# Optimization experiments

Hardware: AMD Instinct MI355X
Metric: run time of the kernel (lower is better)

Reference implementation:

```python
import jax, jax.numpy as jnp
import numpy as np

MAX_SPIKE_TIME = 100.0
TH = 1.0
BIT = 8
K = 3
PAD = 1
OUT_CH = 64


def _unfold3x3(x):
    # torch F.unfold(kernel=3, padding=1, stride=1): output (B, C*9, H*W),
    # feature order channel-major then (kh, kw).
    B, C, H, W = x.shape
    xp = jnp.pad(x, ((0, 0), (0, 0), (PAD, PAD), (PAD, PAD)))
    cols = [xp[:, :, i:i + H, j:j + W] for i in range(K) for j in range(K)]
    p = jnp.stack(cols, axis=2)            # (B, C, 9, H, W)
    return p.reshape(B, C * K * K, H * W)  # (B, C*9, L)


def _weight_quantization(w):
    # tanh -> scale by global abs-max (no grad through alpha) -> round with STE
    w = jnp.tanh(w)
    alpha = jax.lax.stop_gradient(jnp.max(jnp.abs(w)))
    qmax = float(2 ** (BIT - 1) - 1)
    w = jnp.clip(w / alpha, -1.0, 1.0) * qmax
    w_hat = jax.lax.stop_gradient(jnp.round(w) - w) + w
    return w_hat * alpha / qmax


def _t_linear_c(patches, weight):
    # patches: (B, L, F_in); weight: (F_out, F_in)
    sorted_inp = jnp.sort(patches, axis=-1)      # (B, L, F_in)
    indic = jnp.argsort(patches, axis=-1)        # (B, L, F_in)
    wT = weight.T                                # (F_in, F_out)
    w_sorted = wT[indic]                         # (B, L, F_in, F_out)
    wq = _weight_quantization(w_sorted)
    si = sorted_inp[..., None]                   # (B, L, F_in, 1)
    weight_input_mul = si * wq
    weight_sum = jnp.cumsum(wq, axis=-2)
    input_weight_sum = jnp.cumsum(weight_input_mul, axis=-2)
    out_all = input_weight_sum / jnp.clip(weight_sum - TH, 1e-10, 1e10)
    out_spike = jnp.where(weight_sum < TH, MAX_SPIKE_TIME, out_all)
    out_spike = jnp.where(out_spike < si, MAX_SPIKE_TIME, out_spike)
    # causality check against the NEXT sorted input time (1.0 for the last slot)
    next_in = jnp.concatenate([si[..., 1:, :], jnp.ones_like(si[..., :1, :])], axis=-2)
    out_spike = jnp.where(out_spike > next_in, MAX_SPIKE_TIME, out_spike)
    return jnp.min(out_spike, axis=-2)           # (B, L, F_out)


def setup_inputs() -> dict:
    key = jax.random.key(0)
    k1, k2 = jax.random.split(key)
    inp = jax.random.uniform(k1, (4, 16, 32, 32), dtype=jnp.float32)
    in_features = K * K * 16
    weight = jax.random.uniform(k2, (OUT_CH, in_features), dtype=jnp.float32) * (10.0 / in_features)
    return {"inp": inp, "weight": weight}


def reference(inp, weight):
    B, C, H, W = inp.shape
    patches = _unfold3x3(inp).transpose(0, 2, 1)          # (B, L, F_in)
    patches = jnp.where(patches < 0.1, MAX_SPIKE_TIME, patches)
    out = _t_linear_c(patches, weight)                    # (B, L, F_out)
    out = out.transpose(0, 2, 1).reshape(B, OUT_CH, H, W)  # stride=1, pad=1 -> same HW
    return out
```

## Files before the change

kernel.cpp:

```cpp
#include <hip/hip_runtime.h>
#include <math.h>

constexpr int F_IN   = 144;
constexpr int F_OUT  = 64;
constexpr int H_IMG  = 32;
constexpr int W_IMG  = 32;
constexpr int NPIX   = 4 * H_IMG * W_IMG;
constexpr int PPB    = 8;
constexpr int NTHR   = PPB * 64;
#define MAX_SPIKE 100.0f

__global__ __launch_bounds__(256) void quant_fused_kernel(
    const float* __restrict__ w,
    float* __restrict__ wqT)
{
#pragma clang fp contract(off)
    __shared__ float wred[4];
    const int tid = threadIdx.x;

    float m = 0.f;
    {
        const float4* w4 = (const float4*)w;
        for (int i = tid; i < (F_OUT * F_IN) / 4; i += 256) {
            const float4 v = w4[i];
            m = fmaxf(m, fmaxf(fmaxf(fabsf(v.x), fabsf(v.y)),
                               fmaxf(fabsf(v.z), fabsf(v.w))));
        }
    }
    for (int s = 32; s > 0; s >>= 1)
        m = fmaxf(m, __shfl_xor(m, s, 64));
    if ((tid & 63) == 0) wred[tid >> 6] = m;
    __syncthreads();
    const float mw = fmaxf(fmaxf(wred[0], wred[1]), fmaxf(wred[2], wred[3]));
    const float alpha = tanhf(mw);

    const int i = blockIdx.x * 256 + tid;
    const int o = i / F_IN;
    const int f = i - o * F_IN;
    const float t = tanhf(w[i]);
    float x = t / alpha;
    x = fminf(fmaxf(x, -1.f), 1.f) * 127.f;
    const float r = rintf(x);
    wqT[f * F_OUT + o] = r * alpha / 127.f;
}

__global__ __launch_bounds__(NTHR, 4) void spike_conv_kernel(
    const float* __restrict__ inp,
    const float* __restrict__ wq,
    float* __restrict__ out)
{
#pragma clang fp contract(off)
    __shared__ __align__(16) float wql[F_IN * F_OUT];
    __shared__ __align__(16) unsigned long long kr[PPB][F_IN];
    __shared__ float sv[PPB][F_IN + 1];

    const int tid  = threadIdx.x;
    const int lane = tid & 63;
    const int wv_i = tid >> 6;
    const int p    = blockIdx.x * PPB + wv_i;
    const int b    = p >> 10;
    const int l    = p & 1023;
    const int h    = l >> 5;
    const int w    = l & 31;

    for (int c = wv_i; c < 36; c += PPB) {
        const float* g = wq + c * 256 + lane * 4;
        __builtin_amdgcn_global_load_lds(
            (const __attribute__((address_space(1))) void*)g,
            (__attribute__((address_space(3))) void*)&wql[c * 256],
            16, 0, 0);
    }

    float v0f, v1f, v2f;
    unsigned long long key0, key1, key2;
    {
        int idx[3] = { lane, lane + 64, lane + 128 };
        float vals[3];
        for (int m = 0; m < 3; ++m) {
            const int i = idx[m];
            float v = MAX_SPIKE;
            if (i < F_IN) {
                const int c  = i / 9;
                const int r  = i - c * 9;
                const int kh = r / 3;
                const int kw = r - kh * 3;
                const int hh = h + kh - 1;
                const int ww = w + kw - 1;
                float x = 0.f;
                if (hh >= 0 && hh < H_IMG && ww >= 0 && ww < W_IMG)
                    x = inp[((b * 16 + c) * H_IMG + hh) * W_IMG + ww];
                v = (x < 0.1f) ? MAX_SPIKE : x;
                kr[wv_i][i] = ((unsigned long long)__float_as_uint(v) << 8)
                              | (unsigned)i;
            }
            vals[m] = v;
        }
        v0f = vals[0]; v1f = vals[1]; v2f = vals[2];
        key0 = ((unsigned long long)__float_as_uint(v0f) << 8) | (unsigned)idx[0];
        key1 = ((unsigned long long)__float_as_uint(v1f) << 8) | (unsigned)idx[1];
        key2 = ((unsigned long long)__float_as_uint(v2f) << 8) | (unsigned)idx[2];
        if (lane == 0) sv[wv_i][F_IN] = 1.0f;
    }

    int r0 = 0, r1 = 0, r2 = 0;
    {
        const ulonglong2* ks2 = (const ulonglong2*)&kr[wv_i][0];
#pragma unroll 4
        for (int j = 0; j < F_IN / 2; ++j) {
            const ulonglong2 kk = ks2[j];
            r0 += (kk.x < key0) + (kk.y < key0);
            r1 += (kk.x < key1) + (kk.y < key1);
            r2 += (kk.x < key2) + (kk.y < key2);
        }
    }

    {
        unsigned* krlo = (unsigned*)&kr[wv_i][0];
        sv[wv_i][r0] = v0f;  krlo[2 * r0] = (unsigned)lane << 6;
        sv[wv_i][r1] = v1f;  krlo[2 * r1] = (unsigned)(lane + 64) << 6;
        if (lane < F_IN - 128) {
            sv[wv_i][r2] = v2f;  krlo[2 * r2] = (unsigned)(lane + 128) << 6;
        }
    }

    {
        unsigned* krhi = (unsigned*)&kr[wv_i][0];
        for (int k = lane; k < F_IN; k += 64)
            krhi[2 * k + 1] = __float_as_uint(sv[wv_i][k + 1]);
    }

    __syncthreads();

    float s   = sv[wv_i][0];
    float ws  = 0.f;
    float iws = 0.f;
    float mn  = MAX_SPIKE;
    bool  done = false;
    const ulonglong2* rec2 = (const ulonglong2*)&kr[wv_i][0];
    for (int k0 = 0; k0 < F_IN; k0 += 8) {
        if (s >= MAX_SPIKE) break;
        const ulonglong2 ra = rec2[(k0 >> 1) + 0];
        const ulonglong2 rb = rec2[(k0 >> 1) + 1];
        const ulonglong2 rc = rec2[(k0 >> 1) + 2];
        const ulonglong2 rd = rec2[(k0 >> 1) + 3];
        const unsigned long long r8[8] = { ra.x, ra.y, rb.x, rb.y,
                                           rc.x, rc.y, rd.x, rd.y };
        float su[8], nx[8], wsu[8], iwsu[8];
#pragma unroll
        for (int u = 0; u < 8; ++u) {
            su[u] = s;
            nx[u] = __uint_as_float((unsigned)(r8[u] >> 32));
            const float wvv = wql[(unsigned)r8[u] + lane];
            ws += wvv;
            const float prod = su[u] * wvv;
            iws += prod;
            wsu[u]  = ws;
            iwsu[u] = iws;
            s = nx[u];
        }
        if (!__all(wsu[7] < 1.0f)) {
#pragma unroll
            for (int u = 0; u < 8; ++u) {
                const float d = fmaxf(wsu[u] - 1.0f, 1e-10f);
                const float q = iwsu[u] / d;
                const bool valid = (wsu[u] >= 1.0f) & (q >= su[u]) & (q <= nx[u]);
                if (valid & !done) { mn = q; done = true; }
            }
            if (__all(done)) break;
        }
    }
    out[(b * F_OUT + lane) * 1024 + l] = mn;
}

extern "C" void kernel_launch(void* const* d_in, const int* in_sizes, int n_in,
                              void* d_out, int out_size, void* d_ws, size_t ws_size,
                              hipStream_t stream) {
    const float* inp = (const float*)d_in[0];
    const float* w   = (const float*)d_in[1];
    float* out = (float*)d_out;
    float* wqT = (float*)d_ws;

    quant_fused_kernel<<<36, 256, 0, stream>>>(w, wqT);
    spike_conv_kernel<<<NPIX / PPB, NTHR, 0, stream>>>(inp, wqT, out);
}
```

Before: 80.73 us.

## Replace LDS key buffer with cross-lane readlane broadcasts for ranking and scan

The rank-counting sort no longer stores all keys to LDS and rereads them. Each lane's keys are broadcast to the wave with readlane instead. After scattering the sorted records to LDS once, each lane reloads one record per section, builds the next-value neighbour by shuffle, and the serial scan pulls the weight offset and next value via readlane rather than LDS reads. This removes LDS traffic and the second staging pass. The cost is many scalar readlane operations with SGPR-to-VGPR dependencies and less flexible early exit.

```diff
diff --git a/kernel.cpp b/kernel.cpp
--- a/kernel.cpp
+++ b/kernel.cpp
@@ -44,6 +44,67 @@
     wqT[f * F_OUT + o] = r * alpha / 127.f;
 }
 
+__device__ __forceinline__ unsigned rl_u32(unsigned v, int j) {
+    return (unsigned)__builtin_amdgcn_readlane((int)v, j);
+}
+__device__ __forceinline__ float rl_f32(float v, int j) {
+    return __uint_as_float((unsigned)__builtin_amdgcn_readlane(__float_as_int(v), j));
+}
+
+__device__ __forceinline__ void rank_accum(
+    unsigned kh, unsigned kl, int cnt,
+    unsigned long long key0, unsigned long long key1, unsigned long long key2,
+    int& r0, int& r1, int& r2)
+{
+#pragma unroll 4
+    for (int j = 0; j < cnt; ++j) {
+        const unsigned long long kj =
+            ((unsigned long long)rl_u32(kh, j) << 32) | rl_u32(kl, j);
+        r0 += (kj < key0);
+        r1 += (kj < key1);
+        r2 += (kj < key2);
+    }
+}
+
+__device__ __forceinline__ bool scan_section(
+    float nxreg, unsigned ofreg, int cnt, const float* __restrict__ wqlane,
+    float& s, float& ws, float& iws, float& mn, bool& done)
+{
+#pragma clang fp contract(off)
+    for (int j0 = 0; j0 < cnt; j0 += 8) {
+        if (s >= MAX_SPIKE) return true;
+        float nx[8]; const float* wp[8];
+#pragma unroll
+        for (int u = 0; u < 8; ++u) {
+            nx[u] = rl_f32(nxreg, j0 + u);
+            wp[u] = wqlane + rl_u32(ofreg, j0 + u);
+        }
+        float su[8], wsu[8], iwsu[8];
+#pragma unroll
+        for (int u = 0; u < 8; ++u) {
+            su[u] = (u == 0) ? s : nx[u - 1];
+            const float wvv = *wp[u];
+            ws += wvv;
+            const float prod = su[u] * wvv;
+            iws += prod;
+            wsu[u]  = ws;
+            iwsu[u] = iws;
+        }
+        s = nx[7];
+        if (!__all(wsu[7] < 1.0f)) {
+#pragma unroll
+            for (int u = 0; u < 8; ++u) {
+                const float d = fmaxf(wsu[u] - 1.0f, 1e-10f);
+                const float q = iwsu[u] / d;
+                const bool valid = (wsu[u] >= 1.0f) & (q >= su[u]) & (q <= nx[u]);
+                if (valid & !done) { mn = q; done = true; }
+            }
+            if (__all(done)) return true;
+        }
+    }
+    return false;
+}
+
 __global__ __launch_bounds__(NTHR, 4) void spike_conv_kernel(
     const float* __restrict__ inp,
     const float* __restrict__ wq,
@@ -51,8 +112,7 @@
 {
 #pragma clang fp contract(off)
     __shared__ __align__(16) float wql[F_IN * F_OUT];
-    __shared__ __align__(16) unsigned long long kr[PPB][F_IN];
-    __shared__ float sv[PPB][F_IN + 1];
+    __shared__ __align__(16) unsigned long long kr[PPB][192];
 
     const int tid  = threadIdx.x;
     const int lane = tid & 63;
@@ -71,104 +131,81 @@
             16, 0, 0);
     }
 
-    float v0f, v1f, v2f;
-    unsigned long long key0, key1, key2;
+    float vv[3];
+    unsigned long long key[3];
+    unsigned khi[3], klo[3];
+#pragma unroll
+    for (int m = 0; m < 3; ++m) {
+        const int i = lane + 64 * m;
+        float v = MAX_SPIKE;
+        if (i < F_IN) {
+            const int c  = i / 9;
+            const int r  = i - c * 9;
+            const int kh = r / 3;
+            const int kw = r - kh * 3;
+            const int hh = h + kh - 1;
+            const int ww = w + kw - 1;
+            float x = 0.f;
+            if (hh >= 0 && hh < H_IMG && ww >= 0 && ww < W_IMG)
+                x = inp[((b * 16 + c) * H_IMG + hh) * W_IMG + ww];
+            v = (x < 0.1f) ? MAX_SPIKE : x;
+        }
+        vv[m] = v;
+        const unsigned bits = __float_as_uint(v);
+        key[m] = ((unsigned long long)bits << 8) | (unsigned)i;
+        khi[m] = (unsigned)(key[m] >> 32);
+        klo[m] = (unsigned)key[m];
+    }
+
+    int r0 = 0, r1 = 0, r2 = 0;
+    rank_accum(khi[0], klo[0], 64, key[0], key[1], key[2], r0, r1, r2);
+    rank_accum(khi[1], klo[1], 64, key[0], key[1], key[2], r0, r1, r2);
+    rank_accum(khi[2], klo[2], 16, key[0], key[1], key[2], r0, r1, r2);
+
     {
-        int idx[3] = { lane, lane + 64, lane + 128 };
-        float vals[3];
-        for (int m = 0; m < 3; ++m) {
-            const int i = idx[m];
-            float v = MAX_SPIKE;
-            if (i < F_IN) {
-                const int c  = i / 9;
-                const int r  = i - c * 9;
-                const int kh = r / 3;
-                const int kw = r - kh * 3;
-                const int hh = h + kh - 1;
-                const int ww = w + kw - 1;
-                float x = 0.f;
-                if (hh >= 0 && hh < H_IMG && ww >= 0 && ww < W_IMG)
-                    x = inp[((b * 16 + c) * H_IMG + hh) * W_IMG + ww];
-                v = (x < 0.1f) ? MAX_SPIKE : x;
-                kr[wv_i][i] = ((unsigned long long)__float_as_uint(v) << 8)
-                              | (unsigned)i;
-            }
-            vals[m] = v;
-        }
-        v0f = vals[0]; v1f = vals[1]; v2f = vals[2];
-        key0 = ((unsigned long long)__float_as_uint(v0f) << 8) | (unsigned)idx[0];
-        key1 = ((unsigned long long)__float_as_uint(v1f) << 8) | (unsigned)idx[1];
-        key2 = ((unsigned long long)__float_as_uint(v2f) << 8) | (unsigned)idx[2];
-        if (lane == 0) sv[wv_i][F_IN] = 1.0f;
-    }
-
-    int r0 = 0, r1 = 0, r2 = 0;
-    {
-        const ulonglong2* ks2 = (const ulonglong2*)&kr[wv_i][0];
-#pragma unroll 4
-        for (int j = 0; j < F_IN / 2; ++j) {
-            const ulonglong2 kk = ks2[j];
-            r0 += (kk.x < key0) + (kk.y < key0);
-            r1 += (kk.x < key1) + (kk.y < key1);
-            r2 += (kk.x < key2) + (kk.y < key2);
-        }
-    }
-
-    {
-        unsigned* krlo = (unsigned*)&kr[wv_i][0];
-        sv[wv_i][r0] = v0f;  krlo[2 * r0] = (unsigned)lane << 6;
-        sv[wv_i][r1] = v1f;  krlo[2 * r1] = (unsigned)(lane + 64) << 6;
-        if (lane < F_IN - 128) {
-            sv[wv_i][r2] = v2f;  krlo[2 * r2] = (unsigned)(lane + 128) << 6;
-        }
-    }
-
-    {
-        unsigned* krhi = (unsigned*)&kr[wv_i][0];
-        for (int k = lane; k < F_IN; k += 64)
-            krhi[2 * k + 1] = __float_as_uint(sv[wv_i][k + 1]);
-    }
+        unsigned long long* kb = &kr[wv_i][0];
+        kb[r0] = ((unsigned long long)__float_as_uint(vv[0]) << 32)
+                 | ((unsigned)lane << 6);
+        kb[r1] = ((unsigned long long)__float_as_uint(vv[1]) << 32)
+                 | ((unsigned)(lane + 64) << 6);
+        if (lane < F_IN - 128)
+            kb[r2] = ((unsigned long long)__float_as_uint(vv[2]) << 32)
+                     | ((unsigned)(lane + 128) << 6);
+    }
+
+    const unsigned long long rc0 = kr[wv_i][lane];
+    const unsigned long long rc1 = kr[wv_i][lane + 64];
+    const unsigned long long rc2 = kr[wv_i][lane + 128];
+    const float    sv0 = __uint_as_float((unsigned)(rc0 >> 32));
+    const float    sv1 = __uint_as_float((unsigned)(rc1 >> 32));
+    const float    sv2 = __uint_as_float((unsigned)(rc2 >> 32));
+    const unsigned of0 = (unsigned)rc0;
+    const unsigned of1 = (unsigned)rc1;
+    const unsigned of2 = (unsigned)rc2;
+
+    const int nlane = (lane + 1) & 63;
+    float nx0 = __shfl(sv0, nlane);
+    float nx1 = __shfl(sv1, nlane);
+    float nx2 = __shfl(sv2, nlane);
+    const float c1 = __shfl(sv1, 0);
+    const float c2 = __shfl(sv2, 0);
+    if (lane == 63) { nx0 = c1; nx1 = c2; }
+    if (lane == 15) { nx2 = 1.0f; }
+
+    float s = __shfl(sv0, 0);
 
     __syncthreads();
 
-    float s   = sv[wv_i][0];
+    const float* wqlane = wql + lane;
     float ws  = 0.f;
     float iws = 0.f;
     float mn  = MAX_SPIKE;
     bool  done = false;
-    const ulonglong2* rec2 = (const ulonglong2*)&kr[wv_i][0];
-    for (int k0 = 0; k0 < F_IN; k0 += 8) {
-        if (s >= MAX_SPIKE) break;
-        const ulonglong2 ra = rec2[(k0 >> 1) + 0];
-        const ulonglong2 rb = rec2[(k0 >> 1) + 1];
-        const ulonglong2 rc = rec2[(k0 >> 1) + 2];
-        const ulonglong2 rd = rec2[(k0 >> 1) + 3];
-        const unsigned long long r8[8] = { ra.x, ra.y, rb.x, rb.y,
-                                           rc.x, rc.y, rd.x, rd.y };
-        float su[8], nx[8], wsu[8], iwsu[8];
-#pragma unroll
-        for (int u = 0; u < 8; ++u) {
-            su[u] = s;
-            nx[u] = __uint_as_float((unsigned)(r8[u] >> 32));
-            const float wvv = wql[(unsigned)r8[u] + lane];
-            ws += wvv;
-            const float prod = su[u] * wvv;
-            iws += prod;
-            wsu[u]  = ws;
-            iwsu[u] = iws;
-            s = nx[u];
-        }
-        if (!__all(wsu[7] < 1.0f)) {
-#pragma unroll
-            for (int u = 0; u < 8; ++u) {
-                const float d = fmaxf(wsu[u] - 1.0f, 1e-10f);
-                const float q = iwsu[u] / d;
-                const bool valid = (wsu[u] >= 1.0f) & (q >= su[u]) & (q <= nx[u]);
-                if (valid & !done) { mn = q; done = true; }
-            }
-            if (__all(done)) break;
-        }
-    }
+    bool fin;
+    fin = scan_section(nx0, of0, 64, wqlane, s, ws, iws, mn, done);
+    if (!fin) fin = scan_section(nx1, of1, 64, wqlane, s, ws, iws, mn, done);
+    if (!fin) scan_section(nx2, of2, 16, wqlane, s, ws, iws, mn, done);
+
     out[(b * F_OUT + lane) * 1024 + l] = mn;
 }
 
```

New measurement: 88.85 us. 10.1% more time.

## Fuse weight quantization into spike kernel and rank sort keys via wave ballots

Applied to the files above, without the earlier changes.

Drops the separate quantization kernel. Every block now loads the raw weights, reduces the global abs-max across its waves, and writes quantized, transposed weights straight into LDS. The LDS-based rank counting for sorting patch values is replaced by readlane broadcasts and ballot/popcount comparisons, removing the shared-memory key scan. In exchange, each of the 512 blocks redoes the full weight quantization with 18 tanh per thread, which adds redundant transcendental work and global reads.

```diff
diff --git a/kernel.cpp b/kernel.cpp
--- a/kernel.cpp
+++ b/kernel.cpp
@@ -10,49 +10,20 @@
 constexpr int NTHR   = PPB * 64;
 #define MAX_SPIKE 100.0f
 
-__global__ __launch_bounds__(256) void quant_fused_kernel(
-    const float* __restrict__ w,
-    float* __restrict__ wqT)
-{
-#pragma clang fp contract(off)
-    __shared__ float wred[4];
-    const int tid = threadIdx.x;
-
-    float m = 0.f;
-    {
-        const float4* w4 = (const float4*)w;
-        for (int i = tid; i < (F_OUT * F_IN) / 4; i += 256) {
-            const float4 v = w4[i];
-            m = fmaxf(m, fmaxf(fmaxf(fabsf(v.x), fabsf(v.y)),
-                               fmaxf(fabsf(v.z), fabsf(v.w))));
-        }
-    }
-    for (int s = 32; s > 0; s >>= 1)
-        m = fmaxf(m, __shfl_xor(m, s, 64));
-    if ((tid & 63) == 0) wred[tid >> 6] = m;
-    __syncthreads();
-    const float mw = fmaxf(fmaxf(wred[0], wred[1]), fmaxf(wred[2], wred[3]));
-    const float alpha = tanhf(mw);
-
-    const int i = blockIdx.x * 256 + tid;
-    const int o = i / F_IN;
-    const int f = i - o * F_IN;
-    const float t = tanhf(w[i]);
-    float x = t / alpha;
-    x = fminf(fmaxf(x, -1.f), 1.f) * 127.f;
-    const float r = rintf(x);
-    wqT[f * F_OUT + o] = r * alpha / 127.f;
+__device__ __forceinline__ unsigned rl_u32(unsigned v, int j) {
+    return (unsigned)__builtin_amdgcn_readlane((int)v, j);
 }
 
-__global__ __launch_bounds__(NTHR, 4) void spike_conv_kernel(
+__global__ __launch_bounds__(NTHR, 4) void fused_spike_kernel(
     const float* __restrict__ inp,
-    const float* __restrict__ wq,
+    const float* __restrict__ w,
     float* __restrict__ out)
 {
 #pragma clang fp contract(off)
     __shared__ __align__(16) float wql[F_IN * F_OUT];
     __shared__ __align__(16) unsigned long long kr[PPB][F_IN];
     __shared__ float sv[PPB][F_IN + 1];
+    __shared__ float red[PPB];
 
     const int tid  = threadIdx.x;
     const int lane = tid & 63;
@@ -61,65 +32,100 @@
     const int b    = p >> 10;
     const int l    = p & 1023;
     const int h    = l >> 5;
-    const int w    = l & 31;
+    const int wc   = l & 31;
 
-    for (int c = wv_i; c < 36; c += PPB) {
-        const float* g = wq + c * 256 + lane * 4;
-        __builtin_amdgcn_global_load_lds(
-            (const __attribute__((address_space(1))) void*)g,
-            (__attribute__((address_space(3))) void*)&wql[c * 256],
-            16, 0, 0);
+    float wreg[18];
+    float m = 0.f;
+#pragma unroll
+    for (int t = 0; t < 18; ++t) {
+        const int j = tid + 512 * t;
+        const int f = j >> 6;
+        const int o = j & 63;
+        const float x = w[o * F_IN + f];
+        wreg[t] = x;
+        m = fmaxf(m, fabsf(x));
+    }
+    for (int s = 32; s > 0; s >>= 1)
+        m = fmaxf(m, __shfl_xor(m, s, 64));
+    if (lane == 0) red[wv_i] = m;
+
+    float vv[3];
+    unsigned long long k64[3];
+    unsigned khi[3], klo[3];
+#pragma unroll
+    for (int mm = 0; mm < 3; ++mm) {
+        const int i = lane + 64 * mm;
+        float v = MAX_SPIKE;
+        if (i < F_IN) {
+            const int c  = i / 9;
+            const int r  = i - c * 9;
+            const int kh = r / 3;
+            const int kw = r - kh * 3;
+            const int hh = h + kh - 1;
+            const int wg = wc + kw - 1;
+            float x = 0.f;
+            if (hh >= 0 && hh < H_IMG && wg >= 0 && wg < W_IMG)
+                x = inp[((b * 16 + c) * H_IMG + hh) * W_IMG + wg];
+            v = (x < 0.1f) ? MAX_SPIKE : x;
+        }
+        vv[mm] = v;
+        k64[mm] = ((unsigned long long)__float_as_uint(v) << 8) | (unsigned)i;
+        khi[mm] = (unsigned)(k64[mm] >> 32);
+        klo[mm] = (unsigned)k64[mm];
+    }
+    if (lane == 0) sv[wv_i][F_IN] = 1.0f;
+
+    __syncthreads();
+
+    float mw = red[0];
+#pragma unroll
+    for (int t = 1; t < PPB; ++t) mw = fmaxf(mw, red[t]);
+    const float alpha = tanhf(mw);
+#pragma unroll
+    for (int t = 0; t < 18; ++t) {
+        const int j = tid + 512 * t;
+        const float tt = tanhf(wreg[t]);
+        float x = tt / alpha;
+        x = fminf(fmaxf(x, -1.f), 1.f) * 127.f;
+        const float r = rintf(x);
+        wql[j] = r * alpha / 127.f;
     }
 
-    float v0f, v1f, v2f;
-    unsigned long long key0, key1, key2;
-    {
-        int idx[3] = { lane, lane + 64, lane + 128 };
-        float vals[3];
-        for (int m = 0; m < 3; ++m) {
-            const int i = idx[m];
-            float v = MAX_SPIKE;
-            if (i < F_IN) {
-                const int c  = i / 9;
-                const int r  = i - c * 9;
-                const int kh = r / 3;
-                const int kw = r - kh * 3;
-                const int hh = h + kh - 1;
-                const int ww = w + kw - 1;
-                float x = 0.f;
-                if (hh >= 0 && hh < H_IMG && ww >= 0 && ww < W_IMG)
-                    x = inp[((b * 16 + c) * H_IMG + hh) * W_IMG + ww];
-                v = (x < 0.1f) ? MAX_SPIKE : x;
-                kr[wv_i][i] = ((unsigned long long)__float_as_uint(v) << 8)
-                              | (unsigned)i;
-            }
-            vals[m] = v;
-        }
-        v0f = vals[0]; v1f = vals[1]; v2f = vals[2];
-        key0 = ((unsigned long long)__float_as_uint(v0f) << 8) | (unsigned)idx[0];
-        key1 = ((unsigned long long)__float_as_uint(v1f) << 8) | (unsigned)idx[1];
-        key2 = ((unsigned long long)__float_as_uint(v2f) << 8) | (unsigned)idx[2];
-        if (lane == 0) sv[wv_i][F_IN] = 1.0f;
+    int vr0 = 0, vr1 = 0, vr2 = 0;
+#pragma unroll 8
+    for (int j = 0; j < 64; ++j) {
+        const unsigned long long sk =
+            ((unsigned long long)rl_u32(khi[0], j) << 32) | rl_u32(klo[0], j);
+        const int r = (int)(__popcll(__ballot(k64[0] < sk))
+                          + __popcll(__ballot(k64[1] < sk))
+                          + __popcll(__ballot(k64[2] < sk) & 0xFFFFull));
+        vr0 = (lane == j) ? r : vr0;
     }
-
-    int r0 = 0, r1 = 0, r2 = 0;
-    {
-        const ulonglong2* ks2 = (const ulonglong2*)&kr[wv_i][0];
-#pragma unroll 4
-        for (int j = 0; j < F_IN / 2; ++j) {
-            const ulonglong2 kk = ks2[j];
-            r0 += (kk.x < key0) + (kk.y < key0);
-            r1 += (kk.x < key1) + (kk.y < key1);
-            r2 += (kk.x < key2) + (kk.y < key2);
-        }
+#pragma unroll 8
+    for (int j = 0; j < 64; ++j) {
+        const unsigned long long sk =
+            ((unsigned long long)rl_u32(khi[1], j) << 32) | rl_u32(klo[1], j);
+        const int r = (int)(__popcll(__ballot(k64[0] < sk))
+                          + __popcll(__ballot(k64[1] < sk))
+                          + __popcll(__ballot(k64[2] < sk) & 0xFFFFull));
+        vr1 = (lane == j) ? r : vr1;
+    }
+#pragma unroll 8
+    for (int j = 0; j < 16; ++j) {
+        const unsigned long long sk =
+            ((unsigned long long)rl_u32(khi[2], j) << 32) | rl_u32(klo[2], j);
+        const int r = (int)(__popcll(__ballot(k64[0] < sk))
+                          + __popcll(__ballot(k64[1] < sk))
+                          + __popcll(__ballot(k64[2] < sk) & 0xFFFFull));
+        vr2 = (lane == j) ? r : vr2;
     }
 
     {
         unsigned* krlo = (unsigned*)&kr[wv_i][0];
-        sv[wv_i][r0] = v0f;  krlo[2 * r0] = (unsigned)lane << 6;
-        sv[wv_i][r1] = v1f;  krlo[2 * r1] = (unsigned)(lane + 64) << 6;
+        sv[wv_i][vr0] = vv[0];  krlo[2 * vr0] = (unsigned)lane << 6;
+        sv[wv_i][vr1] = vv[1];  krlo[2 * vr1] = (unsigned)(lane + 64) << 6;
         if (lane < F_IN - 128) {
-            sv[wv_i][r2] = v2f;  krlo[2 * r2] = (unsigned)(lane + 128) << 6;
+            sv[wv_i][vr2] = vv[2];  krlo[2 * vr2] = (unsigned)(lane + 128) << 6;
         }
     }
 
@@ -178,8 +184,6 @@
     const float* inp = (const float*)d_in[0];
     const float* w   = (const float*)d_in[1];
     float* out = (float*)d_out;
-    float* wqT = (float*)d_ws;
 
-    quant_fused_kernel<<<36, 256, 0, stream>>>(w, wqT);
-    spike_conv_kernel<<<NPIX / PPB, NTHR, 0, stream>>>(inp, wqT, out);
+    fused_spike_kernel<<<NPIX / PPB, NTHR, 0, stream>>>(inp, w, out);
 }
```

New measurement: 91.71 us. 13.6% more time.
